# Kernel optimization log

Hardware: AMD Instinct MI355X
Metric: run time of the kernel (lower is better)

## Reference

```python
import jax, jax.numpy as jnp
import numpy as np

ALPHA = 0.2          # LeakyReLU negative slope
NEG_INF = -9e15      # mask fill value used by the original module


def setup_inputs() -> dict:
    key = jax.random.key(0)
    k1, k2, k3, k4 = jax.random.split(key, 4)
    N, F_in, F_out = 8192, 256, 64
    h = jax.random.normal(k1, (N, F_in), dtype=jnp.float32)
    adj = jax.random.randint(k2, (N, N), 0, 2).astype(jnp.int32)
    # xavier_uniform with gain=1.414
    gain = 1.414
    bW = gain * np.sqrt(6.0 / (F_in + F_out))
    W = jax.random.uniform(k3, (F_in, F_out), dtype=jnp.float32, minval=-bW, maxval=bW)
    ba = gain * np.sqrt(6.0 / (2 * F_out + 1))
    a = jax.random.uniform(k4, (2 * F_out, 1), dtype=jnp.float32, minval=-ba, maxval=ba)
    return {"h": h, "adj": adj, "W": W, "a": a}


def reference(h, adj, W, a):
    # Wh: [N, F_out]
    Wh = h @ W
    F_out = Wh.shape[1]
    # Decompose a_input @ a: e[i, j] = leakyrelu(Wh[j]@a[:F] + Wh[i]@a[F:])
    # (repeat gives Wh[j] in the first half, repeat_interleave gives Wh[i] in the second)
    f_src = (Wh @ a[:F_out]).reshape(-1)   # [N], coefficient of column index j
    f_dst = (Wh @ a[F_out:]).reshape(-1)   # [N], coefficient of row index i
    e = jax.nn.leaky_relu(f_dst[:, None] + f_src[None, :], negative_slope=ALPHA)  # [N, N]
    attention = jnp.where(adj > 0, e, NEG_INF)
    attention = jax.nn.softmax(attention, axis=1)
    # dropout is identity in eval mode (training=False)
    h_prime = attention @ Wh               # [N, F_out]
    return jax.nn.elu(h_prime)             # concat=True path
```

## Files before the change

### kernel.cpp

```cpp
#include <hip/hip_runtime.h>
#include <hip/hip_bf16.h>

#define GN     8192
#define FIN    256
#define FOUT   64
#define NSPLIT 8
#define JSEG   1024
#define NCH    32
#define PF     4
#define ROWS_B 128
#define LOG2E  1.44269504f

typedef float  f32x4  __attribute__((ext_vector_type(4)));
typedef __bf16 bf16x8 __attribute__((ext_vector_type(8)));
typedef int    iv4    __attribute__((ext_vector_type(4)));

__device__ __forceinline__ unsigned short f2bf_rtne(float x) {
    unsigned int u = __float_as_uint(x);
    unsigned int r = (u + 0x7FFFu + ((u >> 16) & 1u)) >> 16;
    return (unsigned short)r;
}

__global__ __launch_bounds__(256) void k_wh(const float* __restrict__ h,
                                            const float* __restrict__ W,
                                            const float* __restrict__ a,
                                            float* __restrict__ fsrc,
                                            float* __restrict__ fdst,
                                            uint4* __restrict__ whfrag) {
    __shared__ float Wt[FOUT][FIN + 1];
    __shared__ float WhL[32][FOUT + 1];
    int t = threadIdx.x;
    int col = t & 63, kq4 = t >> 6;
#pragma unroll
    for (int rep = 0; rep < 16; ++rep) {
        int k0 = kq4 * 4 + rep * 16;
        float4 wv;
        wv.x = W[(k0 + 0) * FOUT + col];
        wv.y = W[(k0 + 1) * FOUT + col];
        wv.z = W[(k0 + 2) * FOUT + col];
        wv.w = W[(k0 + 3) * FOUT + col];
        *(float4*)&Wt[col][k0] = wv;
    }
    __syncthreads();
    int wave = t >> 6, lane = t & 63;
    float a1 = a[lane], a2 = a[FOUT + lane];
    int bid = blockIdx.x;
#pragma unroll
    for (int rr = 0; rr < 8; ++rr) {
        int il = wave * 8 + rr;
        int i  = bid * 32 + il;
        const float* hrow = h + (size_t)i * FIN;
        float acc = 0.f;
#pragma unroll 8
        for (int k0 = 0; k0 < FIN; k0 += 4) {
            float4 hv = *(const float4*)&hrow[k0];
            float4 wv = *(const float4*)&Wt[lane][k0];
            acc += hv.x * wv.x + hv.y * wv.y + hv.z * wv.z + hv.w * wv.w;
        }
        WhL[il][lane] = acc;
        float v1 = acc * a1, v2 = acc * a2;
#pragma unroll
        for (int off = 32; off > 0; off >>= 1) {
            v1 += __shfl_xor(v1, off);
            v2 += __shfl_xor(v2, off);
        }
        if (lane == 0) {
            fsrc[i] = fminf(v1, 30.f) * LOG2E;
            fdst[i] = fminf(v2, 30.f) * LOG2E;
        }
    }
    __syncthreads();
    int lane2 = t & 63, ct = t >> 6;
    int colc = ct * 16 + (lane2 & 15);
    int gb = lane2 >> 4;
    unsigned int pk[4];
#pragma unroll
    for (int p = 0; p < 4; ++p) {
        int jo = ((p >> 1) * 16) + gb * 4 + (p & 1) * 2;
        unsigned int lo = f2bf_rtne(WhL[jo    ][colc]);
        unsigned int hi = f2bf_rtne(WhL[jo + 1][colc]);
        pk[p] = lo | (hi << 16);
    }
    uint4 o; o.x = pk[0]; o.y = pk[1]; o.z = pk[2]; o.w = pk[3];
    whfrag[(size_t)(bid * 4 + ct) * 64 + lane2] = o;
}

__global__ __launch_bounds__(512, 1) void k_attn(const int* __restrict__ adj,
                                                 const float* __restrict__ fsrc,
                                                 const float* __restrict__ fdst,
                                                 const uint4* __restrict__ whfrag,
                                                 float* __restrict__ pacc,
                                                 float* __restrict__ pden) {
    __shared__ uint4 whL[NCH * 4 * 64];
    __shared__ float fsL[JSEG];

    int t = threadIdx.x, wv = t >> 6, lane = t & 63;
    int bid = blockIdx.x;
    int rt = bid >> 3, q = bid & (NSPLIT - 1);
    int rowbase = rt * ROWS_B;

    {
        const uint4* src = whfrag + (size_t)q * (NCH * 4 * 64);
#pragma unroll
        for (int it = 0; it < 16; ++it) whL[it * 512 + t] = src[it * 512 + t];
        if (t < 256) *(float4*)&fsL[t * 4] = *(const float4*)&fsrc[q * JSEG + t * 4];
    }
    __syncthreads();

    int r = lane & 15, g = lane >> 4;
    int row = rowbase + wv * 16 + r;
    float d = fdst[row];
    const int* arow = adj + (size_t)row * GN + q * JSEG + g * 4;

    f32x4 acc0 = {0.f, 0.f, 0.f, 0.f}, acc1 = acc0, acc2 = acc0, acc3 = acc0;
    float den = 0.f;

    iv4 pfa[PF], pfb[PF];
#pragma unroll
    for (int dd = 0; dd < PF; ++dd) {
        pfa[dd] = *(const iv4*)(arow + dd * 32);
        pfb[dd] = *(const iv4*)(arow + dd * 32 + 16);
    }

    for (int cb = 0; cb < NCH; cb += PF) {
#pragma unroll
        for (int dd = 0; dd < PF; ++dd) {
            int ch = cb + dd;
            int ae[8] = {pfa[dd][0], pfa[dd][1], pfa[dd][2], pfa[dd][3],
                         pfb[dd][0], pfb[dd][1], pfb[dd][2], pfb[dd][3]};
            float4 s0 = *(const float4*)&fsL[ch * 32 + g * 4];
            float4 s1 = *(const float4*)&fsL[ch * 32 + 16 + g * 4];
            float se[8] = {s0.x, s0.y, s0.z, s0.w, s1.x, s1.y, s1.z, s1.w};

            int nch = ch + PF;
            if (nch < NCH) {
                pfa[dd] = *(const iv4*)(arow + nch * 32);
                pfb[dd] = *(const iv4*)(arow + nch * 32 + 16);
            }

            bf16x8 af;
            float ws = 0.f;
#pragma unroll
            for (int e = 0; e < 8; ++e) {
                float ev = d + se[e];
                float lr = fmaxf(ev, 0.2f * ev);
                float ex = __builtin_amdgcn_exp2f(lr);
                float wvv = (ae[e] > 0) ? ex : 0.f;
                ws += wvv;
                af[e] = (__bf16)wvv;
            }
            den += ws;

            const uint4* bl = &whL[(ch * 4) * 64 + lane];
            uint4 b0 = bl[0], b1 = bl[64], b2 = bl[128], b3 = bl[192];
            acc0 = __builtin_amdgcn_mfma_f32_16x16x32_bf16(af, __builtin_bit_cast(bf16x8, b0), acc0, 0, 0, 0);
            acc1 = __builtin_amdgcn_mfma_f32_16x16x32_bf16(af, __builtin_bit_cast(bf16x8, b1), acc1, 0, 0, 0);
            acc2 = __builtin_amdgcn_mfma_f32_16x16x32_bf16(af, __builtin_bit_cast(bf16x8, b2), acc2, 0, 0, 0);
            acc3 = __builtin_amdgcn_mfma_f32_16x16x32_bf16(af, __builtin_bit_cast(bf16x8, b3), acc3, 0, 0, 0);
        }
    }

    den += __shfl_xor(den, 16);
    den += __shfl_xor(den, 32);

    float* po = pacc + (size_t)q * (GN * FOUT);
    int orow = rowbase + wv * 16 + g * 4;
#pragma unroll
    for (int reg = 0; reg < 4; ++reg) {
        po[(size_t)(orow + reg) * FOUT +  0 + r] = acc0[reg];
        po[(size_t)(orow + reg) * FOUT + 16 + r] = acc1[reg];
        po[(size_t)(orow + reg) * FOUT + 32 + r] = acc2[reg];
        po[(size_t)(orow + reg) * FOUT + 48 + r] = acc3[reg];
    }
    if (g == 0) pden[(size_t)q * GN + row] = den;
}

__global__ __launch_bounds__(256) void k_out(const float* __restrict__ pacc,
                                             const float* __restrict__ pden,
                                             float* __restrict__ out) {
    int idx = blockIdx.x * 256 + threadIdx.x;
    int i = idx >> 6;
    float num = 0.f, den = 0.f;
#pragma unroll
    for (int qq = 0; qq < NSPLIT; ++qq) {
        num += pacc[(size_t)qq * (GN * FOUT) + idx];
        den += pden[(size_t)qq * GN + i];
    }
    float v = (den != 0.f) ? num / den : 0.f;
    out[idx] = v > 0.f ? v : __expf(v) - 1.f;
}

extern "C" void kernel_launch(void* const* d_in, const int* in_sizes, int n_in,
                              void* d_out, int out_size, void* d_ws, size_t ws_size,
                              hipStream_t stream) {
    (void)in_sizes; (void)n_in; (void)out_size; (void)ws_size;
    const float* h   = (const float*)d_in[0];
    const int*   adj = (const int*)d_in[1];
    const float* W   = (const float*)d_in[2];
    const float* a   = (const float*)d_in[3];
    float* out = (float*)d_out;

    float* ws     = (float*)d_ws;
    float* fsrc   = ws;
    float* fdst   = fsrc + GN;
    uint4* whfrag = (uint4*)(fdst + GN);
    float* pacc   = (float*)(whfrag + (size_t)GN / 32 * 4 * 64);
    float* pden   = pacc + (size_t)NSPLIT * GN * FOUT;

    k_wh  <<<GN / 32,                 256, 0, stream>>>(h, W, a, fsrc, fdst, whfrag);
    k_attn<<<(GN / ROWS_B) * NSPLIT,  512, 0, stream>>>(adj, fsrc, fdst, whfrag, pacc, pden);
    k_out <<<GN * FOUT / 256,         256, 0, stream>>>(pacc, pden, out);
}
```

Baseline: 105.1 us.

## Fuse attention and epilogue with in-block column split and async adj loads to LDS

```diff
diff --git a/kernel.cpp b/kernel.cpp
--- a/kernel.cpp
+++ b/kernel.cpp
@@ -1,15 +1,10 @@
 #include <hip/hip_runtime.h>
 #include <hip/hip_bf16.h>
 
-#define GN     8192
-#define FIN    256
-#define FOUT   64
-#define NSPLIT 8
-#define JSEG   1024
-#define NCH    32
-#define PF     4
-#define ROWS_B 128
-#define LOG2E  1.44269504f
+#define GN    8192
+#define FIN   256
+#define FOUT  64
+#define LOG2E 1.44269504f
 
 typedef float  f32x4  __attribute__((ext_vector_type(4)));
 typedef __bf16 bf16x8 __attribute__((ext_vector_type(8)));
@@ -19,6 +14,12 @@
     unsigned int u = __float_as_uint(x);
     unsigned int r = (u + 0x7FFFu + ((u >> 16) & 1u)) >> 16;
     return (unsigned short)r;
+}
+
+__device__ __forceinline__ void gload_lds16(const void* g, void* l) {
+    __builtin_amdgcn_global_load_lds(
+        (const __attribute__((address_space(1))) void*)g,
+        (__attribute__((address_space(3))) void*)l, 16, 0, 0);
 }
 
 __global__ __launch_bounds__(256) void k_wh(const float* __restrict__ h,
@@ -85,59 +86,73 @@
     whfrag[(size_t)(bid * 4 + ct) * 64 + lane2] = o;
 }
 
-__global__ __launch_bounds__(512, 1) void k_attn(const int* __restrict__ adj,
-                                                 const float* __restrict__ fsrc,
-                                                 const float* __restrict__ fdst,
-                                                 const uint4* __restrict__ whfrag,
-                                                 float* __restrict__ pacc,
-                                                 float* __restrict__ pden) {
-    __shared__ uint4 whL[NCH * 4 * 64];
-    __shared__ float fsL[JSEG];
+__global__ __launch_bounds__(512, 1) void k_gat(const int* __restrict__ adj,
+                                                const float* __restrict__ fsrc,
+                                                const float* __restrict__ fdst,
+                                                const uint4* __restrict__ whfrag,
+                                                float* __restrict__ out) {
+    __shared__ __align__(16) unsigned char smem[32768 + 65536 + 512];
+    float* fsL  = (float*)smem;
+    int*   abuf = (int*)(smem + 32768);
+    float* redS = (float*)(smem + 32768);
+    float* denS = (float*)(smem + 32768 + 65536);
+
+#define ABUF(bi, slot) (abuf + ((((bi) * 8 + wv) * 4 + (slot)) * 256))
 
     int t = threadIdx.x, wv = t >> 6, lane = t & 63;
-    int bid = blockIdx.x;
-    int rt = bid >> 3, q = bid & (NSPLIT - 1);
-    int rowbase = rt * ROWS_B;
+    int m = wv >> 2, p = wv & 3;
+    int r = lane & 15, g = lane >> 4;
+    int rowbase = blockIdx.x * 32;
+    int row = rowbase + m * 16 + r;
+
+    float d = fdst[row];
+    const int* arow = adj + (size_t)row * GN + g * 4;
 
     {
-        const uint4* src = whfrag + (size_t)q * (NCH * 4 * 64);
-#pragma unroll
-        for (int it = 0; it < 16; ++it) whL[it * 512 + t] = src[it * 512 + t];
-        if (t < 256) *(float4*)&fsL[t * 4] = *(const float4*)&fsrc[q * JSEG + t * 4];
-    }
-    __syncthreads();
-
-    int r = lane & 15, g = lane >> 4;
-    int row = rowbase + wv * 16 + r;
-    float d = fdst[row];
-    const int* arow = adj + (size_t)row * GN + q * JSEG + g * 4;
+        int c0 = p, c1 = p + 4;
+        gload_lds16(arow + c0 * 32,      ABUF(0, 0));
+        gload_lds16(arow + c0 * 32 + 16, ABUF(0, 1));
+        gload_lds16(arow + c1 * 32,      ABUF(0, 2));
+        gload_lds16(arow + c1 * 32 + 16, ABUF(0, 3));
+        const float4* src = (const float4*)fsrc;
+        float4* dst = (float4*)fsL;
+#pragma unroll
+        for (int i = 0; i < 4; ++i) dst[t + i * 512] = src[t + i * 512];
+    }
+    __syncthreads();
 
     f32x4 acc0 = {0.f, 0.f, 0.f, 0.f}, acc1 = acc0, acc2 = acc0, acc3 = acc0;
     float den = 0.f;
 
-    iv4 pfa[PF], pfb[PF];
-#pragma unroll
-    for (int dd = 0; dd < PF; ++dd) {
-        pfa[dd] = *(const iv4*)(arow + dd * 32);
-        pfb[dd] = *(const iv4*)(arow + dd * 32 + 16);
-    }
-
-    for (int cb = 0; cb < NCH; cb += PF) {
-#pragma unroll
-        for (int dd = 0; dd < PF; ++dd) {
-            int ch = cb + dd;
-            int ae[8] = {pfa[dd][0], pfa[dd][1], pfa[dd][2], pfa[dd][3],
-                         pfb[dd][0], pfb[dd][1], pfb[dd][2], pfb[dd][3]};
-            float4 s0 = *(const float4*)&fsL[ch * 32 + g * 4];
-            float4 s1 = *(const float4*)&fsL[ch * 32 + 16 + g * 4];
+    for (int ph = 0; ph < 32; ++ph) {
+        int bi = ph & 1;
+        int c0 = ph * 8 + p, c1 = c0 + 4;
+
+        const uint4* bl0 = whfrag + (size_t)c0 * 256 + lane;
+        const uint4* bl1 = whfrag + (size_t)c1 * 256 + lane;
+        uint4 b00 = bl0[0], b01 = bl0[64], b02 = bl0[128], b03 = bl0[192];
+        uint4 b10 = bl1[0], b11 = bl1[64], b12 = bl1[128], b13 = bl1[192];
+        __builtin_amdgcn_sched_barrier(0);
+
+        if (ph + 1 < 32) {
+            int nb = bi ^ 1, n0 = c0 + 8, n1 = c1 + 8;
+            gload_lds16(arow + n0 * 32,      ABUF(nb, 0));
+            gload_lds16(arow + n0 * 32 + 16, ABUF(nb, 1));
+            gload_lds16(arow + n1 * 32,      ABUF(nb, 2));
+            gload_lds16(arow + n1 * 32 + 16, ABUF(nb, 3));
+        }
+        __builtin_amdgcn_sched_barrier(0);
+
+#pragma unroll
+        for (int cl = 0; cl < 2; ++cl) {
+            int c = cl ? c1 : c0;
+            iv4 alo = *(const iv4*)(ABUF(bi, cl * 2)     + lane * 4);
+            iv4 ahi = *(const iv4*)(ABUF(bi, cl * 2 + 1) + lane * 4);
+            int ae[8] = {alo[0], alo[1], alo[2], alo[3],
+                         ahi[0], ahi[1], ahi[2], ahi[3]};
+            float4 s0 = *(const float4*)&fsL[c * 32 + g * 4];
+            float4 s1 = *(const float4*)&fsL[c * 32 + 16 + g * 4];
             float se[8] = {s0.x, s0.y, s0.z, s0.w, s1.x, s1.y, s1.z, s1.w};
-
-            int nch = ch + PF;
-            if (nch < NCH) {
-                pfa[dd] = *(const iv4*)(arow + nch * 32);
-                pfb[dd] = *(const iv4*)(arow + nch * 32 + 16);
-            }
-
             bf16x8 af;
             float ws = 0.f;
 #pragma unroll
@@ -150,44 +165,47 @@
                 af[e] = (__bf16)wvv;
             }
             den += ws;
-
-            const uint4* bl = &whL[(ch * 4) * 64 + lane];
-            uint4 b0 = bl[0], b1 = bl[64], b2 = bl[128], b3 = bl[192];
-            acc0 = __builtin_amdgcn_mfma_f32_16x16x32_bf16(af, __builtin_bit_cast(bf16x8, b0), acc0, 0, 0, 0);
-            acc1 = __builtin_amdgcn_mfma_f32_16x16x32_bf16(af, __builtin_bit_cast(bf16x8, b1), acc1, 0, 0, 0);
-            acc2 = __builtin_amdgcn_mfma_f32_16x16x32_bf16(af, __builtin_bit_cast(bf16x8, b2), acc2, 0, 0, 0);
-            acc3 = __builtin_amdgcn_mfma_f32_16x16x32_bf16(af, __builtin_bit_cast(bf16x8, b3), acc3, 0, 0, 0);
-        }
+            uint4 q0 = cl ? b10 : b00, q1 = cl ? b11 : b01;
+            uint4 q2 = cl ? b12 : b02, q3 = cl ? b13 : b03;
+            acc0 = __builtin_amdgcn_mfma_f32_16x16x32_bf16(af, __builtin_bit_cast(bf16x8, q0), acc0, 0, 0, 0);
+            acc1 = __builtin_amdgcn_mfma_f32_16x16x32_bf16(af, __builtin_bit_cast(bf16x8, q1), acc1, 0, 0, 0);
+            acc2 = __builtin_amdgcn_mfma_f32_16x16x32_bf16(af, __builtin_bit_cast(bf16x8, q2), acc2, 0, 0, 0);
+            acc3 = __builtin_amdgcn_mfma_f32_16x16x32_bf16(af, __builtin_bit_cast(bf16x8, q3), acc3, 0, 0, 0);
+        }
+        __syncthreads();
     }
 
     den += __shfl_xor(den, 16);
     den += __shfl_xor(den, 32);
-
-    float* po = pacc + (size_t)q * (GN * FOUT);
-    int orow = rowbase + wv * 16 + g * 4;
-#pragma unroll
-    for (int reg = 0; reg < 4; ++reg) {
-        po[(size_t)(orow + reg) * FOUT +  0 + r] = acc0[reg];
-        po[(size_t)(orow + reg) * FOUT + 16 + r] = acc1[reg];
-        po[(size_t)(orow + reg) * FOUT + 32 + r] = acc2[reg];
-        po[(size_t)(orow + reg) * FOUT + 48 + r] = acc3[reg];
-    }
-    if (g == 0) pden[(size_t)q * GN + row] = den;
-}
-
-__global__ __launch_bounds__(256) void k_out(const float* __restrict__ pacc,
-                                             const float* __restrict__ pden,
-                                             float* __restrict__ out) {
-    int idx = blockIdx.x * 256 + threadIdx.x;
-    int i = idx >> 6;
-    float num = 0.f, den = 0.f;
-#pragma unroll
-    for (int qq = 0; qq < NSPLIT; ++qq) {
-        num += pacc[(size_t)qq * (GN * FOUT) + idx];
-        den += pden[(size_t)qq * GN + i];
-    }
-    float v = (den != 0.f) ? num / den : 0.f;
-    out[idx] = v > 0.f ? v : __expf(v) - 1.f;
+    if (lane < 16) denS[(m * 4 + p) * 16 + lane] = den;
+    float* rs = redS + ((size_t)wv * 64 + lane) * 16;
+    *(f32x4*)(rs + 0)  = acc0;
+    *(f32x4*)(rs + 4)  = acc1;
+    *(f32x4*)(rs + 8)  = acc2;
+    *(f32x4*)(rs + 12) = acc3;
+    __syncthreads();
+
+    {
+        int or_ = t >> 4, c4 = (t & 15) * 4;
+        int mm = or_ >> 4, rr = or_ & 15, gg = rr >> 2, reg = rr & 3;
+        float dd = denS[(mm * 4 + 0) * 16 + rr] + denS[(mm * 4 + 1) * 16 + rr]
+                 + denS[(mm * 4 + 2) * 16 + rr] + denS[(mm * 4 + 3) * 16 + rr];
+        float inv = (dd != 0.f) ? 1.f / dd : 0.f;
+        float4 o;
+        float* op = &o.x;
+#pragma unroll
+        for (int cc = 0; cc < 4; ++cc) {
+            int c = c4 + cc, tq = c >> 4, r2 = c & 15;
+            float num = 0.f;
+#pragma unroll
+            for (int pp = 0; pp < 4; ++pp)
+                num += redS[((size_t)(mm * 4 + pp) * 64 + gg * 16 + r2) * 16 + tq * 4 + reg];
+            float v = num * inv;
+            op[cc] = v > 0.f ? v : __expf(v) - 1.f;
+        }
+        *(float4*)&out[(size_t)(rowbase + or_) * FOUT + c4] = o;
+    }
+#undef ABUF
 }
 
 extern "C" void kernel_launch(void* const* d_in, const int* in_sizes, int n_in,
@@ -204,10 +222,7 @@
     float* fsrc   = ws;
     float* fdst   = fsrc + GN;
     uint4* whfrag = (uint4*)(fdst + GN);
-    float* pacc   = (float*)(whfrag + (size_t)GN / 32 * 4 * 64);
-    float* pden   = pacc + (size_t)NSPLIT * GN * FOUT;
-
-    k_wh  <<<GN / 32,                 256, 0, stream>>>(h, W, a, fsrc, fdst, whfrag);
-    k_attn<<<(GN / ROWS_B) * NSPLIT,  512, 0, stream>>>(adj, fsrc, fdst, whfrag, pacc, pden);
-    k_out <<<GN * FOUT / 256,         256, 0, stream>>>(pacc, pden, out);
-}
+
+    k_wh <<<GN / 32, 256, 0, stream>>>(h, W, a, fsrc, fdst, whfrag);
+    k_gat<<<GN / 32, 512, 0, stream>>>(adj, fsrc, fdst, whfrag, out);
+}
```

After: 127.1 us. +20.9%, slower.
